# Kernel tuning notes

Hardware: AMD Instinct MI355X
Metric: run time of the kernel (lower is better)

## Reference

```python
import jax, jax.numpy as jnp
import numpy as np


def setup_inputs() -> dict:
    key = jax.random.key(0)
    ks = jax.random.split(key, 8)
    B, S, V, E, H = 64, 128, 8000, 256, 512
    scale = 0.05
    return {
        "inputs": jax.random.randint(ks[0], (B, S), 0, V, dtype=jnp.int64),
        "embedding": jax.random.normal(ks[1], (V, E), dtype=jnp.float32) * scale,
        "W_ih": jax.random.normal(ks[2], (4 * H, E), dtype=jnp.float32) * scale,
        "W_hh": jax.random.normal(ks[3], (4 * H, H), dtype=jnp.float32) * scale,
        "b_ih": jax.random.normal(ks[4], (4 * H,), dtype=jnp.float32) * scale,
        "b_hh": jax.random.normal(ks[5], (4 * H,), dtype=jnp.float32) * scale,
        "W_cls": jax.random.normal(ks[6], (V, H), dtype=jnp.float32) * scale,
        "b_cls": jax.random.normal(ks[7], (V,), dtype=jnp.float32) * scale,
    }


def reference(inputs, embedding, W_ih, W_hh, b_ih, b_hh, W_cls, b_cls):
    B, S = inputs.shape
    H = W_hh.shape[1]
    x = embedding[inputs]  # (B, S, E)
    # batch the input-to-hidden GEMM across all timesteps
    x_gates = jnp.einsum('bse,ge->bsg', x, W_ih) + b_ih + b_hh  # (B, S, 4H)

    def step(carry, xg):
        h, c = carry
        gates = xg + h @ W_hh.T  # (B, 4H)
        i, f, g, o = jnp.split(gates, 4, axis=-1)  # PyTorch LSTMCell gate order
        i = jax.nn.sigmoid(i)
        f = jax.nn.sigmoid(f)
        g = jnp.tanh(g)
        o = jax.nn.sigmoid(o)
        c = f * c + i * g
        h = o * jnp.tanh(c)
        return (h, c), h

    h0 = jnp.zeros((B, H), dtype=x.dtype)
    c0 = jnp.zeros((B, H), dtype=x.dtype)
    _, hs = jax.lax.scan(step, (h0, c0), jnp.swapaxes(x_gates, 0, 1))  # hs: (S, B, H)
    hidden = jnp.swapaxes(hs, 0, 1)  # (B, S, H)
    logits = jnp.einsum('bsh,vh->bsv', hidden, W_cls) + b_cls  # (B, S, V)
    y = jnp.transpose(logits, (0, 2, 1))  # (B, V, S)
    return jax.nn.log_softmax(y, axis=1)
```

## Files before the change

### kernel.cpp

```cpp
#include <hip/hip_runtime.h>


using u16   = unsigned short;
using u32   = unsigned int;
using u16x8 = __attribute__((ext_vector_type(8))) u16;
using bf16x8 = __attribute__((ext_vector_type(8))) __bf16;
using f32x4 = __attribute__((ext_vector_type(4))) float;

#define NB   64
#define NS   128
#define NV   8000
#define NVP  8192
#define NE   256
#define NH   512
#define NG   2048
#define NBS  8192
#define OUT_BSTRIDE 1024000
#define XG_SSTRIDE  131072

__device__ inline u16 f2bf(float f) {
    unsigned x = __builtin_bit_cast(unsigned, f);
    unsigned r = (x + 0x7FFFu + ((x >> 16) & 1u)) >> 16;
    return (u16)r;
}

__device__ inline bf16x8 ld_frag(const u16* p) {
    u16x8 v = *(const u16x8*)p;
    return __builtin_bit_cast(bf16x8, v);
}

__device__ inline u32 load_llc(const u32* p) {
    u32 v;
    asm volatile("global_load_dword %0, %1, off sc0 sc1\n\t"
                 "s_waitcnt vmcnt(0)"
                 : "=v"(v) : "v"(p) : "memory");
    return v;
}
__device__ inline f32x4 load_llc16(const void* p) {
    f32x4 v;
    asm volatile("global_load_dwordx4 %0, %1, off sc0 sc1\n\t"
                 "s_waitcnt vmcnt(0)"
                 : "=v"(v) : "v"(p) : "memory");
    return v;
}
__device__ inline void store_llc(u32* p, u32 v) {
    asm volatile("global_store_dword %0, %1, off sc0 sc1"
                 :: "v"(p), "v"(v) : "memory");
}
__device__ inline void prefetch16(f32x4& d, const float* p) {
    asm volatile("global_load_dwordx4 %0, %1, off"
                 : "=v"(d) : "v"(p) : "memory");
}

__device__ inline void gload_lds16(const u16* g, u16* l) {
    __builtin_amdgcn_global_load_lds(
        (const __attribute__((address_space(1))) unsigned int*)(const void*)g,
        (__attribute__((address_space(3))) unsigned int*)(void*)l,
        16, 0, 0);
}

__device__ inline void quad_transpose(float v[4], int p) {
    float tb[4];
    #pragma unroll
    for (int q2 = 0; q2 < 4; ++q2) tb[q2] = __shfl_xor(v[q2 ^ 2], 2);
    #pragma unroll
    for (int q2 = 0; q2 < 4; ++q2) v[q2] = (((q2 ^ p) & 2) ? tb[q2] : v[q2]);
    #pragma unroll
    for (int q2 = 0; q2 < 4; ++q2) tb[q2] = __shfl_xor(v[q2 ^ 1], 1);
    #pragma unroll
    for (int q2 = 0; q2 < 4; ++q2) v[q2] = (((q2 ^ p) & 1) ? tb[q2] : v[q2]);
}

__device__ inline float lstm_cell(const float v[4], float& c) {
    float i_ = 1.f / (1.f + __expf(-v[0]));
    float f_ = 1.f / (1.f + __expf(-v[1]));
    float e2 = __expf(2.f * v[2]);
    float g_ = 1.f - 2.f / (e2 + 1.f);
    float o_ = 1.f / (1.f + __expf(-v[3]));
    c = f_ * c + i_ * g_;
    float e2c = __expf(2.f * c);
    return o_ * (1.f - 2.f / (e2c + 1.f));
}

__global__ void cvt_bf16(const float* __restrict__ s, u16* __restrict__ d, int n8) {
    const float4* s4 = (const float4*)s;
    for (int i = blockIdx.x * blockDim.x + threadIdx.x; i < n8;
         i += gridDim.x * blockDim.x) {
        float4 a = s4[2 * i], b = s4[2 * i + 1];
        u16x8 o;
        o[0] = f2bf(a.x); o[1] = f2bf(a.y); o[2] = f2bf(a.z); o[3] = f2bf(a.w);
        o[4] = f2bf(b.x); o[5] = f2bf(b.y); o[6] = f2bf(b.z); o[7] = f2bf(b.w);
        ((u16x8*)d)[i] = o;
    }
}

__global__ __launch_bounds__(256) void k1_xgates(
    const u16* __restrict__ Wih, const u16* __restrict__ emb,
    const int* __restrict__ toks,
    const float* __restrict__ bih, const float* __restrict__ bhh,
    float* __restrict__ xg)
{
    __shared__ u16x8 Al8[512];
    __shared__ u16x8 Bl8[512];
    u16* Al = (u16*)Al8;
    u16* Bl = (u16*)Bl8;

    const int t = threadIdx.x;
    const int lane = t & 63, w = t >> 6;
    const int wm = w >> 1, wn = w & 1;
    const int gtile = blockIdx.y * 128, mtile = blockIdx.x * 128;

    const int r0 = t >> 2, r1 = r0 + 64, q = t & 3;
    const int m0 = mtile + r0, m1 = mtile + r1;
    const int tok0 = toks[(m0 & 63) * NS + (m0 >> 6)];
    const int tok1 = toks[(m1 & 63) * NS + (m1 >> 6)];

    f32x4 acc[4][4];
    for (int i = 0; i < 4; ++i)
        for (int j = 0; j < 4; ++j) acc[i][j] = {0.f, 0.f, 0.f, 0.f};

    const int kc8 = (lane >> 4) * 8;
    for (int kk = 0; kk < 8; ++kk) {
        const int k0 = kk * 32;
        *(u16x8*)&Al[t * 8]         = *(const u16x8*)&Wih[(gtile + r0) * NE + k0 + q * 8];
        *(u16x8*)&Al[(t + 256) * 8] = *(const u16x8*)&Wih[(gtile + r1) * NE + k0 + q * 8];
        *(u16x8*)&Bl[t * 8]         = *(const u16x8*)&emb[tok0 * NE + k0 + q * 8];
        *(u16x8*)&Bl[(t + 256) * 8] = *(const u16x8*)&emb[tok1 * NE + k0 + q * 8];
        __syncthreads();
        bf16x8 af[4], bf[4];
        #pragma unroll
        for (int i = 0; i < 4; ++i) {
            af[i] = ld_frag(&Al[(wm * 64 + i * 16 + (lane & 15)) * 32 + kc8]);
            bf[i] = ld_frag(&Bl[(wn * 64 + i * 16 + (lane & 15)) * 32 + kc8]);
        }
        #pragma unroll
        for (int fi = 0; fi < 4; ++fi)
            #pragma unroll
            for (int fj = 0; fj < 4; ++fj)
                acc[fi][fj] = __builtin_amdgcn_mfma_f32_16x16x32_bf16(
                    af[fi], bf[fj], acc[fi][fj], 0, 0, 0);
        __syncthreads();
    }

    #pragma unroll
    for (int fi = 0; fi < 4; ++fi) {
        const int g0 = gtile + wm * 64 + fi * 16 + ((lane >> 4) << 2);
        const float4 v1 = *(const float4*)&bih[g0];
        const float4 v2 = *(const float4*)&bhh[g0];
        float badd[4] = {v1.x + v2.x, v1.y + v2.y, v1.z + v2.z, v1.w + v2.w};
        #pragma unroll
        for (int fj = 0; fj < 4; ++fj) {
            const int m = mtile + wn * 64 + fj * 16 + (lane & 15);
            const int b = m & 63, s = m >> 6;
            float* dst = &xg[s * XG_SSTRIDE + b];
            #pragma unroll
            for (int r = 0; r < 4; ++r)
                dst[(g0 + r) * 64] = acc[fi][fj][r] + badd[r];
        }
    }
}

#define LSTM_NBLK 64

__global__ __launch_bounds__(512, 2) void k2_lstm(
    const u16* __restrict__ Whh,
    const float* __restrict__ xg,
    u16* __restrict__ hbuf,
    u16* __restrict__ hidden,
    u32* __restrict__ flags)
{
    __shared__ __align__(16) u16 hl[16 * 528];

    const int t = threadIdx.x, lane = t & 63, w = t >> 6;
    const int bg = blockIdx.x >> 3, ug = blockIdx.x & 7;
    const int j = lane & 15;
    const int kc8 = (lane >> 4) * 8;

    const int ubase = ug * 64 + w * 8;
    const int grow0 = (j & 3) * 512 + ubase + (j >> 2);
    const int grow1 = grow0 + 4;

    bf16x8 bw0[16], bw1[16];
    #pragma unroll
    for (int kk = 0; kk < 16; ++kk) {
        bw0[kk] = ld_frag(&Whh[grow0 * NH + kk * 32 + kc8]);
        bw1[kk] = ld_frag(&Whh[grow1 * NH + kk * 32 + kc8]);
    }
    #pragma unroll
    for (int kk = 0; kk < 16; ++kk) {
        f32x4 w0 = __builtin_bit_cast(f32x4, bw0[kk]);
        f32x4 w1 = __builtin_bit_cast(f32x4, bw1[kk]);
        asm volatile("" : "+v"(w0), "+v"(w1));
        bw0[kk] = __builtin_bit_cast(bf16x8, w0);
        bw1[kk] = __builtin_bit_cast(bf16x8, w1);
    }

    {
        u16x8 z = {0, 0, 0, 0, 0, 0, 0, 0};
        *(u16x8*)&hl[(8 + (t >> 6)) * 528 + (t & 63) * 8] = z;
    }

    const int srow = t >> 6, scol = (t & 63) * 8;
    const int soff = (bg * 8 + srow) * NH + scol;
    u16* hl_w = &hl[srow * 528 + scol];

    const int p = lane & 3;
    const int q = (lane >> 2) & 3;
    const int batg = bg * 8 + (lane >> 4) * 4 + p;
    const int un0 = ubase + q;
    const bool act = lane < 32;
    const bool sl = act && ((lane & 4) == 0);

    const int xoff0 = grow0 * 64 + bg * 8 + (lane >> 4) * 4;
    const int xoff1 = grow1 * 64 + bg * 8 + (lane >> 4) * 4;

    f32x4 xv0 = {0, 0, 0, 0}, xv1 = {0, 0, 0, 0};
    f32x4 xn0 = {0, 0, 0, 0}, xn1 = {0, 0, 0, 0};
    if (act) {
        xv0 = *(const f32x4*)&xg[xoff0];
        xv1 = *(const f32x4*)&xg[xoff1];
    }
    float cA = 0.f, cB = 0.f;

    for (int step = 0; step < NS; ++step) {
        if (act && step + 1 < NS) {
            const float* xb = &xg[(step + 1) * XG_SSTRIDE];
            prefetch16(xn0, &xb[xoff0]);
            prefetch16(xn1, &xb[xoff1]);
        }
        if (step > 0 && lane < 8) {
            const u32* fp = &flags[(bg * 8 + lane) * 32];
            while ((int)load_llc(fp) < step) __builtin_amdgcn_s_sleep(1);
        }
        {
            f32x4 hv = load_llc16(&hbuf[(step & 1) * (NB * NH) + soff]);
            *(f32x4*)hl_w = hv;
        }
        __syncthreads();

        f32x4 a00 = {0, 0, 0, 0}, a01 = {0, 0, 0, 0};
        f32x4 a10 = {0, 0, 0, 0}, a11 = {0, 0, 0, 0};
        #pragma unroll
        for (int kk = 0; kk < 16; ++kk) {
            bf16x8 av = *(const bf16x8*)&hl[j * 528 + kk * 32 + kc8];
            if (kk & 1) {
                a01 = __builtin_amdgcn_mfma_f32_16x16x32_bf16(av, bw0[kk], a01, 0, 0, 0);
                a11 = __builtin_amdgcn_mfma_f32_16x16x32_bf16(av, bw1[kk], a11, 0, 0, 0);
            } else {
                a00 = __builtin_amdgcn_mfma_f32_16x16x32_bf16(av, bw0[kk], a00, 0, 0, 0);
                a10 = __builtin_amdgcn_mfma_f32_16x16x32_bf16(av, bw1[kk], a10, 0, 0, 0);
            }
        }

        float v0[4], v1[4];
        #pragma unroll
        for (int r = 0; r < 4; ++r) {
            v0[r] = a00[r] + a01[r] + xv0[r];
            v1[r] = a10[r] + a11[r] + xv1[r];
        }
        quad_transpose(v0, p);
        quad_transpose(v1, p);

        float h0 = lstm_cell(v0, cA);
        float h1 = lstm_cell(v1, cB);
        u32 hb0 = f2bf(h0), hb1 = f2bf(h1);
        u32 o0 = (u32)__shfl_xor((int)hb0, 4);
        u32 o1 = (u32)__shfl_xor((int)hb1, 4);
        u32 pr0 = hb0 | (o0 << 16);
        u32 pr1 = hb1 | (o1 << 16);

        if (sl) {
            u16* hn = hbuf + ((step & 1) ^ 1) * (NB * NH);
            store_llc((u32*)&hn[batg * NH + un0], pr0);
            store_llc((u32*)&hn[batg * NH + un0 + 4], pr1);
        }
        xv0 = xn0; xv1 = xn1;
        __syncthreads();

        if (step + 1 < NS && t == 0)
            store_llc(&flags[blockIdx.x * 32], (u32)(step + 1));

        if (sl) {
            *(u32*)&hidden[(batg * NS + step) * NH + un0] = pr0;
            *(u32*)&hidden[(batg * NS + step) * NH + un0 + 4] = pr1;
        }
    }
}

__global__ __launch_bounds__(256) void k3_cls(
    const u16* __restrict__ Wc, const u16* __restrict__ hid,
    const float* __restrict__ bcls,
    float* __restrict__ out, float* __restrict__ lse)
{
    __shared__ __align__(16) u16 Al[128 * 32];
    __shared__ __align__(16) u16 Bl[128 * 32];
    __shared__ float red[2][128];

    const int t = threadIdx.x;
    const int lane = t & 63, w = t >> 6;
    const int wm = w >> 1, wn = w & 1;
    const int vtile = blockIdx.y * 128, mtile = blockIdx.x * 128;

    const int srow = w * 16 + (lane >> 2);
    const int scol = (lane & 3) * 8;
    const u16* gA = &Wc[(vtile + srow) * NH + scol];
    const u16* gB = &hid[(mtile + srow) * NH + scol];
    u16* lA0 = &Al[(w * 16) * 32];
    u16* lA1 = &Al[(w * 16 + 64) * 32];
    u16* lB0 = &Bl[(w * 16) * 32];
    u16* lB1 = &Bl[(w * 16 + 64) * 32];

    f32x4 acc[4][4];
    for (int i = 0; i < 4; ++i)
        for (int j2 = 0; j2 < 4; ++j2) acc[i][j2] = {0.f, 0.f, 0.f, 0.f};

    const int kc8 = (lane >> 4) * 8;
    for (int kk = 0; kk < 16; ++kk) {
        const int k0 = kk * 32;
        gload_lds16(gA + k0,           lA0);
        gload_lds16(gA + 64 * NH + k0, lA1);
        gload_lds16(gB + k0,           lB0);
        gload_lds16(gB + 64 * NH + k0, lB1);
        __syncthreads();
        bf16x8 af[4], bf[4];
        #pragma unroll
        for (int i = 0; i < 4; ++i) {
            af[i] = ld_frag(&Al[(wm * 64 + i * 16 + (lane & 15)) * 32 + kc8]);
            bf[i] = ld_frag(&Bl[(wn * 64 + i * 16 + (lane & 15)) * 32 + kc8]);
        }
        #pragma unroll
        for (int fi = 0; fi < 4; ++fi)
            #pragma unroll
            for (int fj = 0; fj < 4; ++fj)
                acc[fi][fj] = __builtin_amdgcn_mfma_f32_16x16x32_bf16(
                    af[fi], bf[fj], acc[fi][fj], 0, 0, 0);
        __syncthreads();
    }

    float lsum[4] = {0.f, 0.f, 0.f, 0.f};
    #pragma unroll
    for (int fi = 0; fi < 4; ++fi) {
        const int v0 = vtile + wm * 64 + fi * 16 + ((lane >> 4) << 2);
        const bool vok = (v0 < NV);
        float4 bc = {0.f, 0.f, 0.f, 0.f};
        if (vok) bc = *(const float4*)&bcls[v0];
        #pragma unroll
        for (int fj = 0; fj < 4; ++fj) {
            const int m = mtile + wn * 64 + fj * 16 + (lane & 15);
            const int b = m >> 7, s = m & 127;
            if (vok) {
                float* dst = &out[b * OUT_BSTRIDE + v0 * NS + s];
                float e = 0.f;
                #pragma unroll
                for (int r = 0; r < 4; ++r) {
                    float lg = acc[fi][fj][r] + (&bc.x)[r];
                    dst[r * NS] = lg;
                    e += __expf(lg);
                }
                lsum[fj] += e;
            }
        }
    }
    #pragma unroll
    for (int fj = 0; fj < 4; ++fj) {
        lsum[fj] += __shfl_xor(lsum[fj], 16);
        lsum[fj] += __shfl_xor(lsum[fj], 32);
    }
    if (lane < 16) {
        #pragma unroll
        for (int fj = 0; fj < 4; ++fj)
            red[wm][wn * 64 + fj * 16 + lane] = lsum[fj];
    }
    __syncthreads();
    if (t < 128) {
        const int m = mtile + t;
        atomicAdd(&lse[m], red[0][t] + red[1][t]);
    }
}

__global__ void k4_log(const float* __restrict__ lse, float* __restrict__ ll) {
    int i = blockIdx.x * 256 + threadIdx.x;
    if (i < NBS) ll[i] = logf(lse[i]);
}

__global__ void k5_norm(float* __restrict__ out, const float* __restrict__ ll) {
    const int total4 = NB * NV * NS / 4;
    float4* o4 = (float4*)out;
    for (int i = blockIdx.x * blockDim.x + threadIdx.x; i < total4;
         i += gridDim.x * blockDim.x) {
        const int i4 = i * 4;
        const int b = i4 / OUT_BSTRIDE;
        const int s = (i4 - b * OUT_BSTRIDE) & 127;
        float4 v = o4[i];
        const float4 l = *(const float4*)&ll[b * NS + s];
        v.x -= l.x; v.y -= l.y; v.z -= l.z; v.w -= l.w;
        o4[i] = v;
    }
}

extern "C" void kernel_launch(void* const* d_in, const int* in_sizes, int n_in,
                              void* d_out, int out_size, void* d_ws, size_t ws_size,
                              hipStream_t stream) {
    const int*   toks   = (const int*)d_in[0];
    const float* emb_f  = (const float*)d_in[1];
    const float* Wih_f  = (const float*)d_in[2];
    const float* Whh_f  = (const float*)d_in[3];
    const float* bih    = (const float*)d_in[4];
    const float* bhh    = (const float*)d_in[5];
    const float* Wcls_f = (const float*)d_in[6];
    const float* bcls   = (const float*)d_in[7];
    float* out = (float*)d_out;
    char*  ws  = (char*)d_ws;

    u32*   flags  = (u32*)(ws + 0);
    float* lse    = (float*)(ws + 8192);
    float* loglse = (float*)(ws + 40960);
    u16*   hbuf   = (u16*)(ws + 73728);
    u16*   embb   = (u16*)(ws + 204800);
    u16*   wihb   = (u16*)(ws + 4300800);
    u16*   whhb   = (u16*)(ws + 5349376);
    u16*   wclsb  = (u16*)(ws + 7446528);
    u16*   hidden = (u16*)(ws + 15835136);

    float* xg = out;

    hipMemsetAsync(ws, 0, 204800, stream);
    hipMemsetAsync((char*)wclsb + NV * NH * 2, 0, (NVP - NV) * NH * 2, stream);

    cvt_bf16<<<1024, 256, 0, stream>>>(emb_f,  embb,  NV * NE / 8);
    cvt_bf16<<<256,  256, 0, stream>>>(Wih_f,  wihb,  NG * NE / 8);
    cvt_bf16<<<512,  256, 0, stream>>>(Whh_f,  whhb,  NG * NH / 8);
    cvt_bf16<<<1024, 256, 0, stream>>>(Wcls_f, wclsb, NV * NH / 8);

    k1_xgates<<<dim3(64, 16), 256, 0, stream>>>(wihb, embb, toks, bih, bhh, xg);
    k2_lstm<<<LSTM_NBLK, 512, 0, stream>>>(whhb, xg, hbuf, hidden, flags);
    k3_cls<<<dim3(64, 64), 256, 0, stream>>>(wclsb, hidden, bcls, out, lse);
    k4_log<<<32, 256, 0, stream>>>(lse, loglse);
    k5_norm<<<2048, 256, 0, stream>>>(out, loglse);
}
```

Baseline: 626.4 us.

## Vectorize classifier logit stores and stage logits as bf16 in workspace

Swaps the MFMA operand roles in the classifier GEMM so each lane holds four consecutive sequence positions, letting logits be written as float4 or 4xbf16 vector stores. The log-sum-exp partial reduction is reworked to match the new fragment layout. When the workspace is large enough, logits are written as bf16 to a scratch buffer, and the normalization kernel reads them back and writes the fp32 output. This cuts the intermediate write and read traffic of the large output tensor. The cost is bf16 rounding of the logits, and the fast path depends on the workspace size.

Result: faster. 607.1 us (-3.1%).

```diff
diff --git a/kernel.cpp b/kernel.cpp
--- a/kernel.cpp
+++ b/kernel.cpp
@@ -3,6 +3,7 @@
 
 using u16   = unsigned short;
 using u32   = unsigned int;
+using u16x4 = __attribute__((ext_vector_type(4))) u16;
 using u16x8 = __attribute__((ext_vector_type(8))) u16;
 using bf16x8 = __attribute__((ext_vector_type(8))) __bf16;
 using f32x4 = __attribute__((ext_vector_type(4))) float;
@@ -23,6 +24,10 @@
     unsigned r = (x + 0x7FFFu + ((x >> 16) & 1u)) >> 16;
     return (u16)r;
 }
+__device__ inline float bf2f(u16 x) {
+    u32 u = ((u32)x) << 16;
+    return __builtin_bit_cast(float, u);
+}
 
 __device__ inline bf16x8 ld_frag(const u16* p) {
     u16x8 v = *(const u16x8*)p;
@@ -287,10 +292,12 @@
     }
 }
 
+template <bool PACK16>
 __global__ __launch_bounds__(256) void k3_cls(
     const u16* __restrict__ Wc, const u16* __restrict__ hid,
     const float* __restrict__ bcls,
-    float* __restrict__ out, float* __restrict__ lse)
+    float* __restrict__ outf, u16* __restrict__ outb,
+    float* __restrict__ lse)
 {
     __shared__ __align__(16) u16 Al[128 * 32];
     __shared__ __align__(16) u16 Bl[128 * 32];
@@ -322,54 +329,71 @@
         gload_lds16(gB + k0,           lB0);
         gload_lds16(gB + 64 * NH + k0, lB1);
         __syncthreads();
-        bf16x8 af[4], bf[4];
+        bf16x8 mf[4], vf[4];
         #pragma unroll
         for (int i = 0; i < 4; ++i) {
-            af[i] = ld_frag(&Al[(wm * 64 + i * 16 + (lane & 15)) * 32 + kc8]);
-            bf[i] = ld_frag(&Bl[(wn * 64 + i * 16 + (lane & 15)) * 32 + kc8]);
+            mf[i] = ld_frag(&Bl[(wm * 64 + i * 16 + (lane & 15)) * 32 + kc8]);
+            vf[i] = ld_frag(&Al[(wn * 64 + i * 16 + (lane & 15)) * 32 + kc8]);
         }
         #pragma unroll
         for (int fi = 0; fi < 4; ++fi)
             #pragma unroll
             for (int fj = 0; fj < 4; ++fj)
                 acc[fi][fj] = __builtin_amdgcn_mfma_f32_16x16x32_bf16(
-                    af[fi], bf[fj], acc[fi][fj], 0, 0, 0);
-        __syncthreads();
-    }
-
-    float lsum[4] = {0.f, 0.f, 0.f, 0.f};
-    #pragma unroll
-    for (int fi = 0; fi < 4; ++fi) {
-        const int v0 = vtile + wm * 64 + fi * 16 + ((lane >> 4) << 2);
-        const bool vok = (v0 < NV);
-        float4 bc = {0.f, 0.f, 0.f, 0.f};
-        if (vok) bc = *(const float4*)&bcls[v0];
-        #pragma unroll
-        for (int fj = 0; fj < 4; ++fj) {
-            const int m = mtile + wn * 64 + fj * 16 + (lane & 15);
+                    mf[fi], vf[fj], acc[fi][fj], 0, 0, 0);
+        __syncthreads();
+    }
+
+    float lsum[4][4];
+    #pragma unroll
+    for (int fi = 0; fi < 4; ++fi)
+        #pragma unroll
+        for (int r = 0; r < 4; ++r) lsum[fi][r] = 0.f;
+
+    #pragma unroll
+    for (int fj = 0; fj < 4; ++fj) {
+        const int v = vtile + wn * 64 + fj * 16 + (lane & 15);
+        const bool vok = (v < NV);
+        const float bc = vok ? bcls[v] : 0.f;
+        #pragma unroll
+        for (int fi = 0; fi < 4; ++fi) {
+            const int m = mtile + wm * 64 + fi * 16 + ((lane >> 4) << 2);
             const int b = m >> 7, s = m & 127;
+            float lg[4];
+            #pragma unroll
+            for (int r = 0; r < 4; ++r) {
+                lg[r] = acc[fi][fj][r] + bc;
+                if (vok) lsum[fi][r] += __expf(lg[r]);
+            }
             if (vok) {
-                float* dst = &out[b * OUT_BSTRIDE + v0 * NS + s];
-                float e = 0.f;
-                #pragma unroll
-                for (int r = 0; r < 4; ++r) {
-                    float lg = acc[fi][fj][r] + (&bc.x)[r];
-                    dst[r * NS] = lg;
-                    e += __expf(lg);
+                if (PACK16) {
+                    u16x4 o = {f2bf(lg[0]), f2bf(lg[1]), f2bf(lg[2]), f2bf(lg[3])};
+                    *(u16x4*)&outb[b * OUT_BSTRIDE + v * NS + s] = o;
+                } else {
+                    float4 o = {lg[0], lg[1], lg[2], lg[3]};
+                    *(float4*)&outf[b * OUT_BSTRIDE + v * NS + s] = o;
                 }
-                lsum[fj] += e;
             }
         }
     }
-    #pragma unroll
-    for (int fj = 0; fj < 4; ++fj) {
-        lsum[fj] += __shfl_xor(lsum[fj], 16);
-        lsum[fj] += __shfl_xor(lsum[fj], 32);
-    }
-    if (lane < 16) {
-        #pragma unroll
-        for (int fj = 0; fj < 4; ++fj)
-            red[wm][wn * 64 + fj * 16 + lane] = lsum[fj];
+
+    #pragma unroll
+    for (int fi = 0; fi < 4; ++fi)
+        #pragma unroll
+        for (int r = 0; r < 4; ++r) {
+            float sv = lsum[fi][r];
+            sv += __shfl_xor(sv, 1);
+            sv += __shfl_xor(sv, 2);
+            sv += __shfl_xor(sv, 4);
+            sv += __shfl_xor(sv, 8);
+            lsum[fi][r] = sv;
+        }
+    if ((lane & 15) == 0) {
+        #pragma unroll
+        for (int fi = 0; fi < 4; ++fi)
+            #pragma unroll
+            for (int r = 0; r < 4; ++r)
+                red[wn][wm * 64 + fi * 16 + ((lane >> 4) << 2) + r] = lsum[fi][r];
     }
     __syncthreads();
     if (t < 128) {
@@ -390,10 +414,31 @@
          i += gridDim.x * blockDim.x) {
         const int i4 = i * 4;
         const int b = i4 / OUT_BSTRIDE;
-        const int s = (i4 - b * OUT_BSTRIDE) & 127;
+        const int s = i4 & 127;
         float4 v = o4[i];
         const float4 l = *(const float4*)&ll[b * NS + s];
         v.x -= l.x; v.y -= l.y; v.z -= l.z; v.w -= l.w;
+        o4[i] = v;
+    }
+}
+
+__global__ void k5_bf16(float* __restrict__ out, const u16* __restrict__ lgb,
+                        const float* __restrict__ ll) {
+    const int total4 = NB * NV * NS / 4;
+    float4* o4 = (float4*)out;
+    const u16x4* l4 = (const u16x4*)lgb;
+    for (int i = blockIdx.x * blockDim.x + threadIdx.x; i < total4;
+         i += gridDim.x * blockDim.x) {
+        const int i4 = i * 4;
+        const int b = i4 / OUT_BSTRIDE;
+        const int s = i4 & 127;
+        u16x4 g = l4[i];
+        const float4 l = *(const float4*)&ll[b * NS + s];
+        float4 v;
+        v.x = bf2f(g[0]) - l.x;
+        v.y = bf2f(g[1]) - l.y;
+        v.z = bf2f(g[2]) - l.z;
+        v.w = bf2f(g[3]) - l.w;
         o4[i] = v;
     }
 }
@@ -421,6 +466,8 @@
     u16*   whhb   = (u16*)(ws + 5349376);
     u16*   wclsb  = (u16*)(ws + 7446528);
     u16*   hidden = (u16*)(ws + 15835136);
+    u16*   lgb    = (u16*)(ws + 24223744);
+    const bool bigws = ws_size >= (size_t)24223744 + (size_t)NB * NV * NS * 2;
 
     float* xg = out;
 
@@ -434,7 +481,15 @@
 
     k1_xgates<<<dim3(64, 16), 256, 0, stream>>>(wihb, embb, toks, bih, bhh, xg);
     k2_lstm<<<LSTM_NBLK, 512, 0, stream>>>(whhb, xg, hbuf, hidden, flags);
-    k3_cls<<<dim3(64, 64), 256, 0, stream>>>(wclsb, hidden, bcls, out, lse);
-    k4_log<<<32, 256, 0, stream>>>(lse, loglse);
-    k5_norm<<<2048, 256, 0, stream>>>(out, loglse);
-}
+    if (bigws) {
+        k3_cls<true><<<dim3(64, 64), 256, 0, stream>>>(wclsb, hidden, bcls,
+                                                       out, lgb, lse);
+        k4_log<<<32, 256, 0, stream>>>(lse, loglse);
+        k5_bf16<<<2048, 256, 0, stream>>>(out, lgb, loglse);
+    } else {
+        k3_cls<false><<<dim3(64, 64), 256, 0, stream>>>(wclsb, hidden, bcls,
+                                                        out, lgb, lse);
+        k4_log<<<32, 256, 0, stream>>>(lse, loglse);
+        k5_norm<<<2048, 256, 0, stream>>>(out, loglse);
+    }
+}
```
